# Performance work log

Hardware: AMD Instinct MI355X
Metric: run time of the kernel (lower is better)

The kernel has to match this reference:

```python
import jax, jax.numpy as jnp
import numpy as np
from jax import lax

HEADS = 8
L, B, D, H, V, T = 128, 16, 512, 512, 16000, 32


def setup_inputs() -> dict:
    key = jax.random.key(0)
    ks = jax.random.split(key, 16)
    p = lambda k, shape, fan: (jax.random.normal(k, shape, jnp.float32) * (fan ** -0.5))
    output_len = jnp.sort(jax.random.randint(ks[15], (B,), 1, T + 1))[::-1]
    output_len = output_len.at[0].set(T)  # max(output_len) == T, sorted descending
    return dict(
        memory=jax.random.normal(ks[0], (L, B, D), jnp.float32),
        emb=p(ks[1], (V, H), H),
        Wq=p(ks[2], (2 * H, H), 2 * H), bq=jnp.zeros((H,), jnp.float32),
        Wk=p(ks[3], (D, H), D), bk=jnp.zeros((H,), jnp.float32),
        Wv=p(ks[4], (D, H), D), bv=jnp.zeros((H,), jnp.float32),
        W_ih=p(ks[5], (H, 3 * H), H), b_ih=p(ks[6], (3 * H,), H),
        W_hh=p(ks[7], (H, 3 * H), H), b_hh=p(ks[8], (3 * H,), H),
        Wf=p(ks[9], (H, V), H), bf=jnp.zeros((V,), jnp.float32),
        output_len=output_len.astype(jnp.int32),
        max_output_len=T,
    )


def _forward(memory, emb, Wq, bq, Wk, bk, Wv, bv, W_ih, b_ih, W_hh, b_hh, Wf, bf,
             output_len, max_output_len):
    Lm, bs, _ = memory.shape
    Hh = emb.shape[1]
    dk = Hh // HEADS
    scale = 1.0 / np.sqrt(dk)

    def mha(query):  # query: (1, bs, 2H); recomputes k/v projections each step (faithful)
        qh = (query @ Wq + bq).reshape(1, bs, HEADS, dk).transpose(2, 1, 0, 3)   # (h,b,1,dk)
        kh = (memory @ Wk + bk).reshape(Lm, bs, HEADS, dk).transpose(2, 1, 0, 3)  # (h,b,L,dk)
        vh = (memory @ Wv + bv).reshape(Lm, bs, HEADS, dk).transpose(2, 1, 0, 3)
        score = jax.nn.softmax(jnp.einsum('hbqd,hbkd->hbqk', qh, kh) * scale, axis=-1)
        ctx = jnp.einsum('hbqk,hbkd->hbqd', score, vh)          # (h,b,1,dk)
        ctx = ctx.transpose(2, 1, 0, 3).reshape(1, bs, Hh)       # (1,b,H)
        sc = score.transpose(2, 1, 0, 3).mean(axis=2)            # (1,b,L) mean over heads
        return ctx, sc

    def gru_cell(x, h):  # (bs,H),(bs,H) -> (bs,H); PyTorch GRU equations
        gi = x @ W_ih + b_ih
        gh = h @ W_hh + b_hh
        ir, iz, inn = jnp.split(gi, 3, axis=-1)
        hr, hz, hn = jnp.split(gh, 3, axis=-1)
        r = jax.nn.sigmoid(ir + hr)
        z = jax.nn.sigmoid(iz + hz)
        n = jnp.tanh(inn + r * hn)
        return (1.0 - z) * n + z * h

    def step(carry, i):
        out, hid = carry  # (bs,V), (bs,H)
        embedded = emb[jnp.argmax(out, axis=-1)]                 # (bs,H)
        query = jnp.concatenate([embedded, hid], axis=-1)[None]  # (1,bs,2H)
        ctx, sc = mha(query)
        h_new = gru_cell(ctx[0], hid)
        logits = h_new @ Wf + bf                                 # fc on GRU output
        # masking replaces torch's shrinking-batch slicing (output_len sorted desc)
        active = (i < output_len)[:, None].astype(logits.dtype)
        return (logits, h_new), (logits * active, h_new * active, sc[0] * active)

    init = (jnp.zeros((bs, Wf.shape[1]), memory.dtype), jnp.zeros((bs, Hh), memory.dtype))
    _, (outputs, hiddens, scores) = lax.scan(step, init, jnp.arange(max_output_len))
    return outputs, hiddens, scores


def reference(memory, emb, Wq, bq, Wk, bk, Wv, bv, W_ih, b_ih, W_hh, b_hh, Wf, bf,
              output_len, max_output_len):
    return _forward(memory, emb, Wq, bq, Wk, bk, Wv, bv, W_ih, b_ih, W_hh, b_hh,
                    Wf, bf, output_len, max_output_len)
```

## Files before the change

kernel.cpp:

```cpp
#include <hip/hip_runtime.h>

#define LL 128
#define BB 16
#define HH 512
#define VV 16000
#define TT 32
#define NH 8
#define DK 64

#define WS_K 0
#define WS_V (LL*BB*HH)
#define WS_HID0 (2*LL*BB*HH)
#define WS_HID1 (WS_HID0 + BB*HH)
#define WS_CTX  (WS_HID1 + BB*HH)
#define WS_P    (WS_CTX + BB*HH)
#define WS_G    (WS_P + BB*NH*LL)
#define WS_SLOTS_F (WS_G + 6*BB*HH)

#define OUT_HID_OFF ((size_t)TT*BB*VV)
#define OUT_SC_OFF  (OUT_HID_OFF + (size_t)TT*BB*HH)


__global__ __launch_bounds__(256) void kv_kernel(const float* __restrict__ mem,
        const float* __restrict__ Wk, const float* __restrict__ bk,
        const float* __restrict__ Wv, const float* __restrict__ bv,
        float* __restrict__ ws) {
    int blk = blockIdx.x;
    int rg = blk >> 4, ct = blk & 15;
    int isV = ct >= 8;
    int colbase = (ct & 7) * 64;
    const float* W = isV ? Wv : Wk;
    const float* bias = isV ? bv : bk;
    float* outp = ws + (isV ? WS_V : WS_K);
    int rowbase = rg * 16;
    int tid = threadIdx.x;
    __shared__ float As[16*512];

    const float4* srcp = (const float4*)(mem + (size_t)rowbase*512);
    float4* dstp = (float4*)As;
    #pragma unroll
    for (int i = 0; i < 8; ++i) dstp[tid + 256*i] = srcp[tid + 256*i];

    if (blk == 0) {
        for (int i = tid; i < BB*HH; i += 256) ws[WS_HID0 + i] = 0.f;
        unsigned long long* slots = (unsigned long long*)(ws + WS_SLOTS_F);
        for (int i = tid; i < (TT+1)*BB; i += 256)
            slots[i] = (i < BB) ? 0xFFFFFFFFull : 0ull;
    }
    __syncthreads();

    int cq = tid & 15;
    int rq4 = (tid >> 4) & 3;
    int kq = tid >> 6;
    const float4* As4 = (const float4*)As;
    float acc[4][4];
    #pragma unroll
    for (int i = 0; i < 4; ++i) { acc[i][0]=0.f; acc[i][1]=0.f; acc[i][2]=0.f; acc[i][3]=0.f; }
    const float* wp = W + colbase + cq*4;
    for (int k4 = kq*32; k4 < kq*32 + 32; ++k4) {
        float4 a0 = As4[(rq4*4+0)*128 + k4];
        float4 a1 = As4[(rq4*4+1)*128 + k4];
        float4 a2 = As4[(rq4*4+2)*128 + k4];
        float4 a3 = As4[(rq4*4+3)*128 + k4];
        const float* wrow = wp + (size_t)(4*k4)*512;
        float4 w0 = *(const float4*)(wrow);
        float4 w1 = *(const float4*)(wrow + 512);
        float4 w2 = *(const float4*)(wrow + 1024);
        float4 w3 = *(const float4*)(wrow + 1536);
        #define KV_FMA(ri, A) \
            acc[ri][0] += A.x*w0.x + A.y*w1.x + A.z*w2.x + A.w*w3.x; \
            acc[ri][1] += A.x*w0.y + A.y*w1.y + A.z*w2.y + A.w*w3.y; \
            acc[ri][2] += A.x*w0.z + A.y*w1.z + A.z*w2.z + A.w*w3.z; \
            acc[ri][3] += A.x*w0.w + A.y*w1.w + A.z*w2.w + A.w*w3.w;
        KV_FMA(0, a0) KV_FMA(1, a1) KV_FMA(2, a2) KV_FMA(3, a3)
        #undef KV_FMA
    }
    __syncthreads();
    float* red = As;
    #pragma unroll
    for (int ri = 0; ri < 4; ++ri)
        *(float4*)(red + ((rq4*4+ri)*16 + cq)*16 + kq*4) =
            make_float4(acc[ri][0], acc[ri][1], acc[ri][2], acc[ri][3]);
    __syncthreads();
    {
        int c4 = tid & 15, row = tid >> 4;
        float4 b4v = *(const float4*)(bias + colbase + c4*4);
        float o[4] = {b4v.x, b4v.y, b4v.z, b4v.w};
        #pragma unroll
        for (int kq2 = 0; kq2 < 4; ++kq2) {
            const float* pr = red + (row*16 + c4)*16 + kq2*4;
            o[0] += pr[0]; o[1] += pr[1]; o[2] += pr[2]; o[3] += pr[3];
        }
        *(float4*)(outp + (size_t)(rowbase + row)*512 + colbase + c4*4) =
            make_float4(o[0], o[1], o[2], o[3]);
    }
}

__global__ __launch_bounds__(256) void attn_kernel(
        const float* __restrict__ emb, const float* __restrict__ Wq,
        const float* __restrict__ bq, float* __restrict__ ws, int t) {
    int b = blockIdx.x >> 3, h = blockIdx.x & 7;
    int tid = threadIdx.x;
    const float* hid = ws + ((t & 1) ? WS_HID1 : WS_HID0);
    unsigned long long* slots = (unsigned long long*)(ws + WS_SLOTS_F);
    __shared__ float q[2*HH];
    __shared__ float part[8*64];
    __shared__ float qh[64];
    __shared__ float sp[2*LL];
    __shared__ float p[LL];
    __shared__ float cpart[4*64];

    unsigned long long slot = slots[t*BB + b];
    unsigned idx = 0xFFFFFFFFu - (unsigned)(slot & 0xFFFFFFFFull);
    for (int i = tid; i < HH; i += 256) {
        q[i] = emb[(size_t)idx*HH + i];
        q[HH + i] = hid[b*HH + i];
    }
    __syncthreads();

    {
        int c2 = tid & 31, kc = tid >> 5;
        const float* wp = Wq + (size_t)(kc*128)*HH + h*64 + c2*2;
        const float* qp = q + kc*128;
        float a0 = 0.f, a1 = 0.f;
        #pragma unroll 8
        for (int kk = 0; kk < 128; ++kk) {
            float x = qp[kk];
            float2 w2 = *(const float2*)(wp + (size_t)kk*HH);
            a0 += x*w2.x; a1 += x*w2.y;
        }
        part[kc*64 + c2*2]     = a0;
        part[kc*64 + c2*2 + 1] = a1;
    }
    __syncthreads();
    if (tid < 64) {
        float s = bq[h*64 + tid];
        #pragma unroll
        for (int kc = 0; kc < 8; ++kc) s += part[kc*64 + tid];
        qh[tid] = s;
    }
    __syncthreads();

    {
        int l = tid & 127, jh = tid >> 7;
        const float4* kr = (const float4*)(ws + WS_K + ((size_t)(l*BB + b))*HH + h*DK) + jh*8;
        const float4* q4 = (const float4*)qh + jh*8;
        float acc = 0.f;
        #pragma unroll
        for (int j = 0; j < 8; ++j) {
            float4 kv = kr[j], qq = q4[j];
            acc += qq.x*kv.x + qq.y*kv.y + qq.z*kv.z + qq.w*kv.w;
        }
        sp[jh*128 + l] = acc;
    }
    __syncthreads();

    if (tid < 64) {
        float s0 = (sp[tid]      + sp[128 + tid]) * 0.125f;
        float s1 = (sp[64 + tid] + sp[192 + tid]) * 0.125f;
        float m = fmaxf(s0, s1);
        #pragma unroll
        for (int off = 32; off; off >>= 1) m = fmaxf(m, __shfl_xor(m, off));
        float e0 = expf(s0 - m), e1 = expf(s1 - m);
        float sum = e0 + e1;
        #pragma unroll
        for (int off = 32; off; off >>= 1) sum += __shfl_xor(sum, off);
        float inv = 1.f / sum;
        p[tid]      = e0 * inv;
        p[64 + tid] = e1 * inv;
    }
    __syncthreads();
    if (tid < 128) ws[WS_P + (size_t)(b*NH + h)*LL + tid] = p[tid];

    {
        int c = tid & 63, lc = tid >> 6;
        const float* Vp = ws + WS_V + h*DK + c;
        float acc = 0.f;
        #pragma unroll 8
        for (int li = 0; li < 32; ++li) {
            int l = lc*32 + li;
            acc += p[l] * Vp[(size_t)(l*BB + b)*HH];
        }
        cpart[lc*64 + c] = acc;
    }
    __syncthreads();
    if (tid < 64)
        ws[WS_CTX + b*HH + h*DK + tid] =
            cpart[tid] + cpart[64+tid] + cpart[128+tid] + cpart[192+tid];
}

__global__ __launch_bounds__(512) void gates_kernel(
        const float* __restrict__ Wih, const float* __restrict__ Whh,
        const int* __restrict__ olen, float* __restrict__ ws,
        float* __restrict__ out, int t) {
    int blk = blockIdx.x;
    int gcb = blk >> 4, cb = blk & 15;
    int tid = threadIdx.x;
    const float* hid = ws + ((t & 1) ? WS_HID1 : WS_HID0);
    int g = gcb - (gcb >= 3 ? 3 : 0);
    const float* W = (gcb >= 3) ? Whh : Wih;
    const float* src = (gcb >= 3) ? hid : (ws + WS_CTX);
    __shared__ float xs[512*20];
    __shared__ float part[16*512];

    for (int i = tid; i < BB*HH; i += 512) {
        int bb = i >> 9, k = i & 511;
        xs[k*20 + bb] = src[i];
    }
    if (gcb == 0 && tid < 128) {
        float s = 0.f;
        #pragma unroll
        for (int hh = 0; hh < NH; ++hh)
            s += ws[WS_P + (size_t)(cb*NH + hh)*LL + tid];
        bool active = t < olen[cb];
        out[OUT_SC_OFF + ((size_t)t*BB + cb)*LL + tid] = active ? s*0.125f : 0.f;
    }
    __syncthreads();

    int c4 = tid & 7, b4 = (tid >> 3) & 3, kc = tid >> 5;
    const float* wp = W + (size_t)g*HH + cb*32 + c4*4;
    float acc[4][4];
    #pragma unroll
    for (int i = 0; i < 4; ++i) { acc[i][0]=0.f; acc[i][1]=0.f; acc[i][2]=0.f; acc[i][3]=0.f; }
    #pragma unroll 4
    for (int kk = 0; kk < 32; ++kk) {
        int k = kc*32 + kk;
        float4 w4 = *(const float4*)(wp + (size_t)k*(3*HH));
        float4 x4 = *(const float4*)(xs + k*20 + b4*4);
        acc[0][0] += x4.x*w4.x; acc[0][1] += x4.x*w4.y; acc[0][2] += x4.x*w4.z; acc[0][3] += x4.x*w4.w;
        acc[1][0] += x4.y*w4.x; acc[1][1] += x4.y*w4.y; acc[1][2] += x4.y*w4.z; acc[1][3] += x4.y*w4.w;
        acc[2][0] += x4.z*w4.x; acc[2][1] += x4.z*w4.y; acc[2][2] += x4.z*w4.z; acc[2][3] += x4.z*w4.w;
        acc[3][0] += x4.w*w4.x; acc[3][1] += x4.w*w4.y; acc[3][2] += x4.w*w4.z; acc[3][3] += x4.w*w4.w;
    }
    #pragma unroll
    for (int bi = 0; bi < 4; ++bi)
        *(float4*)(part + kc*512 + (b4*4+bi)*32 + c4*4) =
            make_float4(acc[bi][0], acc[bi][1], acc[bi][2], acc[bi][3]);
    __syncthreads();
    {
        int e = tid;
        float s = 0.f;
        #pragma unroll
        for (int kc2 = 0; kc2 < 16; ++kc2) s += part[kc2*512 + e];
        int bb = e >> 5, cc = e & 31;
        ws[WS_G + (size_t)gcb*BB*HH + bb*HH + cb*32 + cc] = s;
    }
}

__global__ __launch_bounds__(256) void logits_kernel(
        const float* __restrict__ Wf, const float* __restrict__ bf,
        const float* __restrict__ bih, const float* __restrict__ bhh,
        const int* __restrict__ olen, float* __restrict__ ws,
        float* __restrict__ out, int t) {
    __shared__ float hs[HH*20];
    __shared__ float red2[4*1028];
    __shared__ unsigned long long am[BB*16];
    int tid = threadIdx.x;
    const float* hold = ws + ((t & 1) ? WS_HID1 : WS_HID0);
    float* hnew_ws = ws + ((t & 1) ? WS_HID0 : WS_HID1);
    const float* gp = ws + WS_G;

    #pragma unroll 2
    for (int jj = 0; jj < 8; ++jj) {
        int u = tid + 256*jj;
        int c = u & 511, bq = u >> 9;
        float hv[4];
        #pragma unroll
        for (int i = 0; i < 4; ++i) {
            int b = bq*4 + i;
            int e = b*HH + c;
            float gir = gp[e],            giz = gp[BB*HH + e],   gin = gp[2*BB*HH + e];
            float ghr = gp[3*BB*HH + e],  ghz = gp[4*BB*HH + e],  ghn = gp[5*BB*HH + e];
            float xr = gir + bih[c]        + ghr + bhh[c];
            float xz = giz + bih[HH + c]   + ghz + bhh[HH + c];
            float r = 1.f/(1.f + __expf(-xr));
            float z = 1.f/(1.f + __expf(-xz));
            float xn = gin + bih[2*HH + c] + r*(ghn + bhh[2*HH + c]);
            float n = 1.f - 2.f/(__expf(2.f*xn) + 1.f);
            float h0 = hold[e];
            float hn2 = (1.f - z)*n + z*h0;
            hv[i] = hn2;
            if (blockIdx.x == 0) {
                hnew_ws[e] = hn2;
                out[OUT_HID_OFF + ((size_t)t*BB + b)*HH + c] = (t < olen[b]) ? hn2 : 0.f;
            }
        }
        *(float4*)(hs + c*20 + bq*4) = make_float4(hv[0], hv[1], hv[2], hv[3]);
    }
    __syncthreads();

    int c8 = tid & 7, bh = (tid >> 3) & 1, kc = tid >> 4;
    int colbase = blockIdx.x * 64;
    float acc[8][8];
    #pragma unroll
    for (int bi = 0; bi < 8; ++bi)
        #pragma unroll
        for (int ci = 0; ci < 8; ++ci) acc[bi][ci] = 0.f;
    const float* wp = Wf + (size_t)kc*VV + colbase + c8*8;
    const float* hp = hs + kc*20 + bh*8;
    #pragma unroll 4
    for (int i = 0; i < 32; ++i) {
        float4 w0 = *(const float4*)(wp);
        float4 w1 = *(const float4*)(wp + 4);
        float4 ha = *(const float4*)(hp);
        float4 hb = *(const float4*)(hp + 4);
        wp += (size_t)16 * VV;
        hp += 16 * 20;
        #define LG_ROW(bi, hc) \
            acc[bi][0] += hc*w0.x; acc[bi][1] += hc*w0.y; acc[bi][2] += hc*w0.z; acc[bi][3] += hc*w0.w; \
            acc[bi][4] += hc*w1.x; acc[bi][5] += hc*w1.y; acc[bi][6] += hc*w1.z; acc[bi][7] += hc*w1.w;
        LG_ROW(0, ha.x) LG_ROW(1, ha.y) LG_ROW(2, ha.z) LG_ROW(3, ha.w)
        LG_ROW(4, hb.x) LG_ROW(5, hb.y) LG_ROW(6, hb.z) LG_ROW(7, hb.w)
        #undef LG_ROW
    }

    #pragma unroll
    for (int bi = 0; bi < 8; ++bi)
        #pragma unroll
        for (int ci = 0; ci < 8; ++ci) {
            float v = acc[bi][ci];
            v += __shfl_xor(v, 16);
            v += __shfl_xor(v, 32);
            acc[bi][ci] = v;
        }
    int wv = tid >> 6;
    if (((tid >> 4) & 3) == 0) {
        #pragma unroll
        for (int bi = 0; bi < 8; ++bi) {
            int b = bh*8 + bi;
            *(float4*)(red2 + wv*1028 + b*64 + c8*8) =
                make_float4(acc[bi][0], acc[bi][1], acc[bi][2], acc[bi][3]);
            *(float4*)(red2 + wv*1028 + b*64 + c8*8 + 4) =
                make_float4(acc[bi][4], acc[bi][5], acc[bi][6], acc[bi][7]);
        }
    }
    __syncthreads();

    {
        int b = tid >> 4, c4 = (tid & 15) * 4;
        float4 s = *(const float4*)(bf + colbase + c4);
        #pragma unroll
        for (int w = 0; w < 4; ++w) {
            float4 r = *(const float4*)(red2 + w*1028 + b*64 + c4);
            s.x += r.x; s.y += r.y; s.z += r.z; s.w += r.w;
        }
        bool active = t < olen[b];
        float4 outv;
        outv.x = active ? s.x : 0.f; outv.y = active ? s.y : 0.f;
        outv.z = active ? s.z : 0.f; outv.w = active ? s.w : 0.f;
        *(float4*)(out + ((size_t)t*BB + b)*VV + colbase + c4) = outv;

        float vals[4] = {s.x, s.y, s.z, s.w};
        unsigned long long m = 0ull;
        #pragma unroll
        for (int j = 0; j < 4; ++j) {
            unsigned u = __float_as_uint(vals[j]);
            u = (u & 0x80000000u) ? ~u : (u | 0x80000000u);
            unsigned col = (unsigned)(colbase + c4 + j);
            unsigned long long e = ((unsigned long long)u << 32)
                                 | (unsigned long long)(0xFFFFFFFFu - col);
            m = e > m ? e : m;
        }
        am[b*16 + (tid & 15)] = m;
    }
    __syncthreads();
    if (tid < BB) {
        unsigned long long m = 0ull;
        #pragma unroll
        for (int i = 0; i < 16; ++i) {
            unsigned long long v = am[tid*16 + i];
            m = v > m ? v : m;
        }
        unsigned long long* slots = (unsigned long long*)(ws + WS_SLOTS_F);
        atomicMax(&slots[(size_t)(t+1)*BB + tid], m);
    }
}

extern "C" void kernel_launch(void* const* d_in, const int* in_sizes, int n_in,
                              void* d_out, int out_size, void* d_ws, size_t ws_size,
                              hipStream_t stream) {
    const float* mem = (const float*)d_in[0];
    const float* emb = (const float*)d_in[1];
    const float* Wq  = (const float*)d_in[2];
    const float* bq  = (const float*)d_in[3];
    const float* Wk  = (const float*)d_in[4];
    const float* bk  = (const float*)d_in[5];
    const float* Wv  = (const float*)d_in[6];
    const float* bv  = (const float*)d_in[7];
    const float* Wih = (const float*)d_in[8];
    const float* bih = (const float*)d_in[9];
    const float* Whh = (const float*)d_in[10];
    const float* bhh = (const float*)d_in[11];
    const float* Wf  = (const float*)d_in[12];
    const float* bf  = (const float*)d_in[13];
    const int* olen  = (const int*)d_in[14];
    float* out = (float*)d_out;
    float* ws  = (float*)d_ws;

    hipLaunchKernelGGL(kv_kernel, dim3(2048), dim3(256), 0, stream, mem, Wk, bk, Wv, bv, ws);
    for (int t = 0; t < TT; ++t) {
        hipLaunchKernelGGL(attn_kernel, dim3(BB*NH), dim3(256), 0, stream, emb, Wq, bq, ws, t);
        hipLaunchKernelGGL(gates_kernel, dim3(96), dim3(512), 0, stream, Wih, Whh, olen, ws, out, t);
        hipLaunchKernelGGL(logits_kernel, dim3(250), dim3(256), 0, stream,
                           Wf, bf, bih, bhh, olen, ws, out, t);
    }
}
```

Baseline: 1.538 ms.

## Fuse GRU elementwise into gates kernel, retile logits and pad KV smem

The GRU nonlinearity moves out of the logits kernel into the gates kernel. Each of 32 blocks now computes all six gate matmuls for 16 columns and writes the new hidden state, plus a transposed copy for the logits kernel to load. Before, every one of the 250 logits blocks recomputed the full GRU update from six gate buffers. The logits kernel is retiled to 500 blocks of 32 columns with all 16 batches per thread, and the KV kernel pads its shared-memory rows and reorders the reduction layout to reduce bank conflicts. The cost is fewer, longer gates blocks that each stream weights serially across six gates.

```diff
diff --git a/kernel.cpp b/kernel.cpp
--- a/kernel.cpp
+++ b/kernel.cpp
@@ -14,8 +14,8 @@
 #define WS_HID1 (WS_HID0 + BB*HH)
 #define WS_CTX  (WS_HID1 + BB*HH)
 #define WS_P    (WS_CTX + BB*HH)
-#define WS_G    (WS_P + BB*NH*LL)
-#define WS_SLOTS_F (WS_G + 6*BB*HH)
+#define WS_HS   (WS_P + BB*NH*LL)
+#define WS_SLOTS_F (WS_HS + 6*BB*HH)
 
 #define OUT_HID_OFF ((size_t)TT*BB*VV)
 #define OUT_SC_OFF  (OUT_HID_OFF + (size_t)TT*BB*HH)
@@ -34,13 +34,18 @@
     float* outp = ws + (isV ? WS_V : WS_K);
     int rowbase = rg * 16;
     int tid = threadIdx.x;
-    __shared__ float As[16*512];
-
-    const float4* srcp = (const float4*)(mem + (size_t)rowbase*512);
-    float4* dstp = (float4*)As;
-    #pragma unroll
-    for (int i = 0; i < 8; ++i) dstp[tid + 256*i] = srcp[tid + 256*i];
-
+    __shared__ float As[16*516];
+
+    {
+        const float4* srcp = (const float4*)(mem + (size_t)rowbase*512);
+        #pragma unroll
+        for (int j = 0; j < 8; ++j) {
+            int i = tid + 256*j;
+            float4 v = srcp[i];
+            int row = i >> 7, c4i = i & 127;
+            *(float4*)(As + row*516 + c4i*4) = v;
+        }
+    }
     if (blk == 0) {
         for (int i = tid; i < BB*HH; i += 256) ws[WS_HID0 + i] = 0.f;
         unsigned long long* slots = (unsigned long long*)(ws + WS_SLOTS_F);
@@ -52,16 +57,15 @@
     int cq = tid & 15;
     int rq4 = (tid >> 4) & 3;
     int kq = tid >> 6;
-    const float4* As4 = (const float4*)As;
     float acc[4][4];
     #pragma unroll
     for (int i = 0; i < 4; ++i) { acc[i][0]=0.f; acc[i][1]=0.f; acc[i][2]=0.f; acc[i][3]=0.f; }
     const float* wp = W + colbase + cq*4;
     for (int k4 = kq*32; k4 < kq*32 + 32; ++k4) {
-        float4 a0 = As4[(rq4*4+0)*128 + k4];
-        float4 a1 = As4[(rq4*4+1)*128 + k4];
-        float4 a2 = As4[(rq4*4+2)*128 + k4];
-        float4 a3 = As4[(rq4*4+3)*128 + k4];
+        float4 a0 = *(const float4*)(As + (rq4*4+0)*516 + k4*4);
+        float4 a1 = *(const float4*)(As + (rq4*4+1)*516 + k4*4);
+        float4 a2 = *(const float4*)(As + (rq4*4+2)*516 + k4*4);
+        float4 a3 = *(const float4*)(As + (rq4*4+3)*516 + k4*4);
         const float* wrow = wp + (size_t)(4*k4)*512;
         float4 w0 = *(const float4*)(wrow);
         float4 w1 = *(const float4*)(wrow + 512);
@@ -79,16 +83,17 @@
     float* red = As;
     #pragma unroll
     for (int ri = 0; ri < 4; ++ri)
-        *(float4*)(red + ((rq4*4+ri)*16 + cq)*16 + kq*4) =
+        *(float4*)(red + ri*1024 + tid*4) =
             make_float4(acc[ri][0], acc[ri][1], acc[ri][2], acc[ri][3]);
     __syncthreads();
     {
         int c4 = tid & 15, row = tid >> 4;
+        int rq = row >> 2, ri = row & 3;
         float4 b4v = *(const float4*)(bias + colbase + c4*4);
         float o[4] = {b4v.x, b4v.y, b4v.z, b4v.w};
         #pragma unroll
         for (int kq2 = 0; kq2 < 4; ++kq2) {
-            const float* pr = red + (row*16 + c4)*16 + kq2*4;
+            const float* pr = red + ri*1024 + (kq2*64 + rq*16 + c4)*4;
             o[0] += pr[0]; o[1] += pr[1]; o[2] += pr[2]; o[3] += pr[3];
         }
         *(float4*)(outp + (size_t)(rowbase + row)*512 + colbase + c4*4) =
@@ -190,178 +195,192 @@
 }
 
 __global__ __launch_bounds__(512) void gates_kernel(
-        const float* __restrict__ Wih, const float* __restrict__ Whh,
+        const float* __restrict__ Wih, const float* __restrict__ bih,
+        const float* __restrict__ Whh, const float* __restrict__ bhh,
         const int* __restrict__ olen, float* __restrict__ ws,
         float* __restrict__ out, int t) {
-    int blk = blockIdx.x;
-    int gcb = blk >> 4, cb = blk & 15;
+    int cb = blockIdx.x;
     int tid = threadIdx.x;
-    const float* hid = ws + ((t & 1) ? WS_HID1 : WS_HID0);
-    int g = gcb - (gcb >= 3 ? 3 : 0);
-    const float* W = (gcb >= 3) ? Whh : Wih;
-    const float* src = (gcb >= 3) ? hid : (ws + WS_CTX);
+    const float* hid_in = ws + ((t & 1) ? WS_HID1 : WS_HID0);
+    float* hid_out = ws + ((t & 1) ? WS_HID0 : WS_HID1);
+    const float* ctx = ws + WS_CTX;
     __shared__ float xs[512*20];
-    __shared__ float part[16*512];
+    __shared__ float hh[512*20];
+    __shared__ float part[8*256];
+    __shared__ float gacc[6*256];
 
     for (int i = tid; i < BB*HH; i += 512) {
         int bb = i >> 9, k = i & 511;
-        xs[k*20 + bb] = src[i];
-    }
-    if (gcb == 0 && tid < 128) {
+        xs[k*20 + bb] = ctx[i];
+        hh[k*20 + bb] = hid_in[i];
+    }
+    if (tid < 64) {
+        int e = cb*64 + tid;
+        int b = e >> 7, l = e & 127;
         float s = 0.f;
         #pragma unroll
-        for (int hh = 0; hh < NH; ++hh)
-            s += ws[WS_P + (size_t)(cb*NH + hh)*LL + tid];
-        bool active = t < olen[cb];
-        out[OUT_SC_OFF + ((size_t)t*BB + cb)*LL + tid] = active ? s*0.125f : 0.f;
-    }
-    __syncthreads();
-
-    int c4 = tid & 7, b4 = (tid >> 3) & 3, kc = tid >> 5;
-    const float* wp = W + (size_t)g*HH + cb*32 + c4*4;
-    float acc[4][4];
-    #pragma unroll
-    for (int i = 0; i < 4; ++i) { acc[i][0]=0.f; acc[i][1]=0.f; acc[i][2]=0.f; acc[i][3]=0.f; }
-    #pragma unroll 4
-    for (int kk = 0; kk < 32; ++kk) {
-        int k = kc*32 + kk;
-        float4 w4 = *(const float4*)(wp + (size_t)k*(3*HH));
-        float4 x4 = *(const float4*)(xs + k*20 + b4*4);
-        acc[0][0] += x4.x*w4.x; acc[0][1] += x4.x*w4.y; acc[0][2] += x4.x*w4.z; acc[0][3] += x4.x*w4.w;
-        acc[1][0] += x4.y*w4.x; acc[1][1] += x4.y*w4.y; acc[1][2] += x4.y*w4.z; acc[1][3] += x4.y*w4.w;
-        acc[2][0] += x4.z*w4.x; acc[2][1] += x4.z*w4.y; acc[2][2] += x4.z*w4.z; acc[2][3] += x4.z*w4.w;
-        acc[3][0] += x4.w*w4.x; acc[3][1] += x4.w*w4.y; acc[3][2] += x4.w*w4.z; acc[3][3] += x4.w*w4.w;
-    }
-    #pragma unroll
-    for (int bi = 0; bi < 4; ++bi)
-        *(float4*)(part + kc*512 + (b4*4+bi)*32 + c4*4) =
-            make_float4(acc[bi][0], acc[bi][1], acc[bi][2], acc[bi][3]);
-    __syncthreads();
-    {
-        int e = tid;
-        float s = 0.f;
-        #pragma unroll
-        for (int kc2 = 0; kc2 < 16; ++kc2) s += part[kc2*512 + e];
-        int bb = e >> 5, cc = e & 31;
-        ws[WS_G + (size_t)gcb*BB*HH + bb*HH + cb*32 + cc] = s;
+        for (int hq = 0; hq < NH; ++hq)
+            s += ws[WS_P + (size_t)(b*NH + hq)*LL + l];
+        out[OUT_SC_OFF + ((size_t)t*BB + b)*LL + l] = (t < olen[b]) ? s*0.125f : 0.f;
+    }
+    __syncthreads();
+
+    int c4 = tid & 3, b4 = (tid >> 2) & 3, kc = tid >> 4;
+    int wv = tid >> 6;
+    for (int g = 0; g < 6; ++g) {
+        const float* W = (g < 3) ? Wih : Whh;
+        int gg = (g < 3) ? g : g - 3;
+        const float* xsrc = (g < 3) ? xs : hh;
+        const float* wp = W + (size_t)kc*(3*HH) + gg*HH + cb*16 + c4*4;
+        const float* xp = xsrc + kc*20 + b4*4;
+        float acc[4][4];
+        #pragma unroll
+        for (int i = 0; i < 4; ++i) { acc[i][0]=0.f; acc[i][1]=0.f; acc[i][2]=0.f; acc[i][3]=0.f; }
+        #pragma unroll 8
+        for (int i = 0; i < 16; ++i) {
+            float4 w4 = *(const float4*)wp;
+            float4 x4 = *(const float4*)xp;
+            wp += (size_t)32*(3*HH);
+            xp += 32*20;
+            acc[0][0] += x4.x*w4.x; acc[0][1] += x4.x*w4.y; acc[0][2] += x4.x*w4.z; acc[0][3] += x4.x*w4.w;
+            acc[1][0] += x4.y*w4.x; acc[1][1] += x4.y*w4.y; acc[1][2] += x4.y*w4.z; acc[1][3] += x4.y*w4.w;
+            acc[2][0] += x4.z*w4.x; acc[2][1] += x4.z*w4.y; acc[2][2] += x4.z*w4.z; acc[2][3] += x4.z*w4.w;
+            acc[3][0] += x4.w*w4.x; acc[3][1] += x4.w*w4.y; acc[3][2] += x4.w*w4.z; acc[3][3] += x4.w*w4.w;
+        }
+        #pragma unroll
+        for (int bi = 0; bi < 4; ++bi)
+            #pragma unroll
+            for (int ci = 0; ci < 4; ++ci) {
+                float v = acc[bi][ci];
+                v += __shfl_xor(v, 16);
+                v += __shfl_xor(v, 32);
+                acc[bi][ci] = v;
+            }
+        if ((tid & 48) == 0) {
+            #pragma unroll
+            for (int bi = 0; bi < 4; ++bi)
+                *(float4*)(part + wv*256 + (b4*4+bi)*16 + c4*4) =
+                    make_float4(acc[bi][0], acc[bi][1], acc[bi][2], acc[bi][3]);
+        }
+        __syncthreads();
+        if (tid < 256) {
+            int b = tid >> 4, c = tid & 15;
+            float s = 0.f;
+            #pragma unroll
+            for (int w = 0; w < 8; ++w) s += part[w*256 + b*16 + c];
+            gacc[g*256 + b*16 + c] = s;
+        }
+        __syncthreads();
+    }
+
+    if (tid < 256) {
+        int b = tid >> 4, c = tid & 15;
+        int col = cb*16 + c;
+        float gir = gacc[0*256 + b*16 + c] + bih[col];
+        float giz = gacc[1*256 + b*16 + c] + bih[HH + col];
+        float gin = gacc[2*256 + b*16 + c] + bih[2*HH + col];
+        float ghr = gacc[3*256 + b*16 + c] + bhh[col];
+        float ghz = gacc[4*256 + b*16 + c] + bhh[HH + col];
+        float ghn = gacc[5*256 + b*16 + c] + bhh[2*HH + col];
+        float r = 1.f/(1.f + __expf(-(gir + ghr)));
+        float z = 1.f/(1.f + __expf(-(giz + ghz)));
+        float xn = gin + r*ghn;
+        float n = 1.f - 2.f/(__expf(2.f*xn) + 1.f);
+        float hprev = hh[col*20 + b];
+        float hnew = (1.f - z)*n + z*hprev;
+        hid_out[b*HH + col] = hnew;
+        out[OUT_HID_OFF + ((size_t)t*BB + b)*HH + col] = (t < olen[b]) ? hnew : 0.f;
+        ws[WS_HS + col*16 + b] = hnew;
     }
 }
 
 __global__ __launch_bounds__(256) void logits_kernel(
         const float* __restrict__ Wf, const float* __restrict__ bf,
-        const float* __restrict__ bih, const float* __restrict__ bhh,
         const int* __restrict__ olen, float* __restrict__ ws,
         float* __restrict__ out, int t) {
     __shared__ float hs[HH*20];
-    __shared__ float red2[4*1028];
+    __shared__ float red[4*512];
     __shared__ unsigned long long am[BB*16];
     int tid = threadIdx.x;
-    const float* hold = ws + ((t & 1) ? WS_HID1 : WS_HID0);
-    float* hnew_ws = ws + ((t & 1) ? WS_HID0 : WS_HID1);
-    const float* gp = ws + WS_G;
-
-    #pragma unroll 2
-    for (int jj = 0; jj < 8; ++jj) {
-        int u = tid + 256*jj;
-        int c = u & 511, bq = u >> 9;
-        float hv[4];
-        #pragma unroll
-        for (int i = 0; i < 4; ++i) {
-            int b = bq*4 + i;
-            int e = b*HH + c;
-            float gir = gp[e],            giz = gp[BB*HH + e],   gin = gp[2*BB*HH + e];
-            float ghr = gp[3*BB*HH + e],  ghz = gp[4*BB*HH + e],  ghn = gp[5*BB*HH + e];
-            float xr = gir + bih[c]        + ghr + bhh[c];
-            float xz = giz + bih[HH + c]   + ghz + bhh[HH + c];
-            float r = 1.f/(1.f + __expf(-xr));
-            float z = 1.f/(1.f + __expf(-xz));
-            float xn = gin + bih[2*HH + c] + r*(ghn + bhh[2*HH + c]);
-            float n = 1.f - 2.f/(__expf(2.f*xn) + 1.f);
-            float h0 = hold[e];
-            float hn2 = (1.f - z)*n + z*h0;
-            hv[i] = hn2;
-            if (blockIdx.x == 0) {
-                hnew_ws[e] = hn2;
-                out[OUT_HID_OFF + ((size_t)t*BB + b)*HH + c] = (t < olen[b]) ? hn2 : 0.f;
-            }
-        }
-        *(float4*)(hs + c*20 + bq*4) = make_float4(hv[0], hv[1], hv[2], hv[3]);
-    }
-    __syncthreads();
-
-    int c8 = tid & 7, bh = (tid >> 3) & 1, kc = tid >> 4;
-    int colbase = blockIdx.x * 64;
-    float acc[8][8];
+
+    {
+        const float4* s4 = (const float4*)(ws + WS_HS);
+        #pragma unroll
+        for (int j = 0; j < 8; ++j) {
+            int i = tid + 256*j;
+            float4 v = s4[i];
+            int row = i >> 2, qo = i & 3;
+            *(float4*)(hs + row*20 + qo*4) = v;
+        }
+    }
+    __syncthreads();
+
+    int c4 = tid & 7, kc = tid >> 3;
+    int colbase = blockIdx.x * 32;
+    float acc[16][4];
     #pragma unroll
-    for (int bi = 0; bi < 8; ++bi)
-        #pragma unroll
-        for (int ci = 0; ci < 8; ++ci) acc[bi][ci] = 0.f;
-    const float* wp = Wf + (size_t)kc*VV + colbase + c8*8;
-    const float* hp = hs + kc*20 + bh*8;
-    #pragma unroll 4
-    for (int i = 0; i < 32; ++i) {
-        float4 w0 = *(const float4*)(wp);
-        float4 w1 = *(const float4*)(wp + 4);
-        float4 ha = *(const float4*)(hp);
-        float4 hb = *(const float4*)(hp + 4);
-        wp += (size_t)16 * VV;
-        hp += 16 * 20;
-        #define LG_ROW(bi, hc) \
-            acc[bi][0] += hc*w0.x; acc[bi][1] += hc*w0.y; acc[bi][2] += hc*w0.z; acc[bi][3] += hc*w0.w; \
-            acc[bi][4] += hc*w1.x; acc[bi][5] += hc*w1.y; acc[bi][6] += hc*w1.z; acc[bi][7] += hc*w1.w;
-        LG_ROW(0, ha.x) LG_ROW(1, ha.y) LG_ROW(2, ha.z) LG_ROW(3, ha.w)
-        LG_ROW(4, hb.x) LG_ROW(5, hb.y) LG_ROW(6, hb.z) LG_ROW(7, hb.w)
-        #undef LG_ROW
+    for (int bi = 0; bi < 16; ++bi) { acc[bi][0]=0.f; acc[bi][1]=0.f; acc[bi][2]=0.f; acc[bi][3]=0.f; }
+    const float* wp = Wf + (size_t)kc*VV + colbase + c4*4;
+    const float* hp = hs + kc*20;
+    #pragma unroll 8
+    for (int i = 0; i < 16; ++i) {
+        float4 w4 = *(const float4*)wp;
+        float4 h0 = *(const float4*)(hp);
+        float4 h1 = *(const float4*)(hp + 4);
+        float4 h2 = *(const float4*)(hp + 8);
+        float4 h3 = *(const float4*)(hp + 12);
+        wp += (size_t)32 * VV;
+        hp += 32 * 20;
+        #define LACC(bi, hv) acc[bi][0] += (hv)*w4.x; acc[bi][1] += (hv)*w4.y; \
+                             acc[bi][2] += (hv)*w4.z; acc[bi][3] += (hv)*w4.w;
+        LACC(0,h0.x)  LACC(1,h0.y)  LACC(2,h0.z)  LACC(3,h0.w)
+        LACC(4,h1.x)  LACC(5,h1.y)  LACC(6,h1.z)  LACC(7,h1.w)
+        LACC(8,h2.x)  LACC(9,h2.y)  LACC(10,h2.z) LACC(11,h2.w)
+        LACC(12,h3.x) LACC(13,h3.y) LACC(14,h3.z) LACC(15,h3.w)
+        #undef LACC
     }
 
     #pragma unroll
-    for (int bi = 0; bi < 8; ++bi)
-        #pragma unroll
-        for (int ci = 0; ci < 8; ++ci) {
+    for (int bi = 0; bi < 16; ++bi)
+        #pragma unroll
+        for (int ci = 0; ci < 4; ++ci) {
             float v = acc[bi][ci];
+            v += __shfl_xor(v, 8);
             v += __shfl_xor(v, 16);
             v += __shfl_xor(v, 32);
             acc[bi][ci] = v;
         }
     int wv = tid >> 6;
-    if (((tid >> 4) & 3) == 0) {
-        #pragma unroll
-        for (int bi = 0; bi < 8; ++bi) {
-            int b = bh*8 + bi;
-            *(float4*)(red2 + wv*1028 + b*64 + c8*8) =
+    if ((tid & 56) == 0) {
+        #pragma unroll
+        for (int bi = 0; bi < 16; ++bi)
+            *(float4*)(red + wv*512 + bi*32 + c4*4) =
                 make_float4(acc[bi][0], acc[bi][1], acc[bi][2], acc[bi][3]);
-            *(float4*)(red2 + wv*1028 + b*64 + c8*8 + 4) =
-                make_float4(acc[bi][4], acc[bi][5], acc[bi][6], acc[bi][7]);
-        }
-    }
-    __syncthreads();
-
-    {
-        int b = tid >> 4, c4 = (tid & 15) * 4;
-        float4 s = *(const float4*)(bf + colbase + c4);
+    }
+    __syncthreads();
+
+    {
+        int b = tid >> 4, cp = (tid & 15) * 2;
+        float2 bf2 = *(const float2*)(bf + colbase + cp);
+        float v0 = bf2.x, v1 = bf2.y;
         #pragma unroll
         for (int w = 0; w < 4; ++w) {
-            float4 r = *(const float4*)(red2 + w*1028 + b*64 + c4);
-            s.x += r.x; s.y += r.y; s.z += r.z; s.w += r.w;
+            v0 += red[w*512 + b*32 + cp];
+            v1 += red[w*512 + b*32 + cp + 1];
         }
         bool active = t < olen[b];
-        float4 outv;
-        outv.x = active ? s.x : 0.f; outv.y = active ? s.y : 0.f;
-        outv.z = active ? s.z : 0.f; outv.w = active ? s.w : 0.f;
-        *(float4*)(out + ((size_t)t*BB + b)*VV + colbase + c4) = outv;
-
-        float vals[4] = {s.x, s.y, s.z, s.w};
-        unsigned long long m = 0ull;
-        #pragma unroll
-        for (int j = 0; j < 4; ++j) {
-            unsigned u = __float_as_uint(vals[j]);
-            u = (u & 0x80000000u) ? ~u : (u | 0x80000000u);
-            unsigned col = (unsigned)(colbase + c4 + j);
-            unsigned long long e = ((unsigned long long)u << 32)
-                                 | (unsigned long long)(0xFFFFFFFFu - col);
-            m = e > m ? e : m;
-        }
-        am[b*16 + (tid & 15)] = m;
+        float2 ov; ov.x = active ? v0 : 0.f; ov.y = active ? v1 : 0.f;
+        *(float2*)(out + ((size_t)t*BB + b)*VV + colbase + cp) = ov;
+
+        unsigned u0 = __float_as_uint(v0);
+        u0 = (u0 & 0x80000000u) ? ~u0 : (u0 | 0x80000000u);
+        unsigned u1 = __float_as_uint(v1);
+        u1 = (u1 & 0x80000000u) ? ~u1 : (u1 | 0x80000000u);
+        unsigned long long e0 = ((unsigned long long)u0 << 32)
+                              | (unsigned long long)(0xFFFFFFFFu - (unsigned)(colbase + cp));
+        unsigned long long e1 = ((unsigned long long)u1 << 32)
+                              | (unsigned long long)(0xFFFFFFFFu - (unsigned)(colbase + cp + 1));
+        am[b*16 + (tid & 15)] = e0 > e1 ? e0 : e1;
     }
     __syncthreads();
     if (tid < BB) {
@@ -400,8 +419,9 @@
     hipLaunchKernelGGL(kv_kernel, dim3(2048), dim3(256), 0, stream, mem, Wk, bk, Wv, bv, ws);
     for (int t = 0; t < TT; ++t) {
         hipLaunchKernelGGL(attn_kernel, dim3(BB*NH), dim3(256), 0, stream, emb, Wq, bq, ws, t);
-        hipLaunchKernelGGL(gates_kernel, dim3(96), dim3(512), 0, stream, Wih, Whh, olen, ws, out, t);
-        hipLaunchKernelGGL(logits_kernel, dim3(250), dim3(256), 0, stream,
-                           Wf, bf, bih, bhh, olen, ws, out, t);
+        hipLaunchKernelGGL(gates_kernel, dim3(32), dim3(512), 0, stream,
+                           Wih, bih, Whh, bhh, olen, ws, out, t);
+        hipLaunchKernelGGL(logits_kernel, dim3(500), dim3(256), 0, stream,
+                           Wf, bf, olen, ws, out, t);
     }
 }
```

Result: faster. 1.463 ms (-4.9%).
